# Kernel optimization log

Measured on AMD Instinct MI355X. Metric: run time of the kernel, lower is better.

Reference implementation:

```python
import jax, jax.numpy as jnp
import numpy as np

B, WK, HRS = 2048, 52, 8760
DT = 0.125          # Euler step in days (3-hourly), exactly representable
RANGE_PRED = 7      # forecast horizon in days


def setup_inputs() -> dict:
    key = jax.random.key(0)
    k1, k2, k3, k4 = jax.random.split(key, 4)
    # X_in: [B, weeks, 5, 1]; channel 0 = start time in days (same across batch,
    # the torch code reads X_in[0, week, 0, 0]); channels 1..4 = N,P,Z,D init.
    X_in = jax.random.uniform(k1, (B, WK, 5, 1), jnp.float32, 0.1, 3.0)
    t0 = jnp.arange(WK, dtype=jnp.float32) * 7.0
    X_in = X_in.at[:, :, 0, 0].set(jnp.broadcast_to(t0, (B, WK)))
    global_f = jax.random.uniform(k2, (B, HRS), jnp.float32)          # light forcing in [0,1]
    global_m = jax.random.uniform(k3, (B, HRS), jnp.float32) * 0.1    # mixing rate, small
    params_value = jax.random.uniform(k4, (B, 10), jnp.float32, 0.1, 1.0)
    return {"X_in": X_in, "global_f": global_f, "global_m": global_m,
            "params_value": params_value, "dt": DT, "range_pred": RANGE_PRED}


def reference(X_in, global_f, global_m, params_value, dt, range_pred):
    # Fixed multipliers from the torch code
    pv = jnp.asarray([1.0, 2.0, 0.1, 0.05, 0.1, 0.3, 0.6, 0.15, 0.4, 0.1], X_in.dtype)
    Q0, Vm, thr = 8.0, 1.0, 0.01  # Q0 = 4 + 2.5 + 1.5 + 0
    chi, rho, gam, lam, eps, alp, bet, eta, phi, zet = [params_value[:, i][:, None] for i in range(10)]  # [B,1]

    n_steps = int(round(range_pred / dt))      # 56
    stride = int(round(1.0 / dt))              # 8 -> daily sampling of output

    # Hourly forcing gather: same time axis for every batch element (torch uses X_in[0,...])
    t0 = X_in[0, :, 0, 0]                                                     # [W]
    times = t0[:, None] + jnp.arange(n_steps + 1, dtype=X_in.dtype) * dt      # [W, S]
    idx = jnp.round(times * 24.0).astype(jnp.int32)
    f = jnp.take(global_f, idx, axis=1)[:, :, :n_steps]                       # [B, W, T]
    m = jnp.take(global_m, idx, axis=1)[:, :, :n_steps]

    def step(carry, ft_mt):
        N, P, Z, D = carry                      # each [B, W]
        ft, mt = ft_mt
        Pc = jnp.maximum(thr, P)
        Zc = jnp.maximum(thr, Z)
        gN = N / (chi * pv[0] + N)
        zg = rho * pv[1] * (1.0 - jnp.exp(-lam * pv[3] * Pc)) * Zc
        up = Vm * gN * ft * Pc
        Nn = N + dt * (-up + alp * pv[5] * zg + eps * pv[4] * P + gam * pv[2] * Z + phi * pv[8] * D + mt * (Q0 - N))
        Pn = P + dt * (up - zg - eps * pv[4] * P - eta * pv[7] * P - mt * P)
        Zn = Z + dt * (bet * pv[6] * zg - gam * pv[2] * Z - mt * Z)
        Dn = D + dt * (eta * pv[7] * P + (1.0 - alp * pv[5] - bet * pv[6]) * zg - phi * pv[8] * D - zet * pv[9] * D - mt * D)
        new = (Nn, Pn, Zn, Dn)
        return new, jnp.stack(new, axis=0)      # [4, B, W]

    carry0 = (X_in[:, :, 1, 0], X_in[:, :, 2, 0], X_in[:, :, 3, 0], X_in[:, :, 4, 0])
    _, ys = jax.lax.scan(step, carry0, (jnp.moveaxis(f, 2, 0), jnp.moveaxis(m, 2, 0)))  # ys: [T, 4, B, W]
    traj = jnp.concatenate([jnp.stack(carry0, axis=0)[None], ys], axis=0)               # [S, 4, B, W]
    out = jnp.moveaxis(traj, (0, 1), (3, 2))                                            # [B, W, 4, S]
    return out[:, :, :, ::stride]               # daily samples: [B, W, 4, range_pred+1]
```

## Files before the change

kernel.cpp:

```cpp
#include <hip/hip_runtime.h>
#include <hip/hip_bf16.h>


typedef float f32x4 __attribute__((ext_vector_type(4)));

#define NPZD_B 2048
#define NPZD_WK 52
#define NPZD_HRS 8760
#define NPZD_NSTEPS 56
#define NPZD_NF4 2190
#define NPZD_WSTRIDE 60
#define NPZD_LDSW (NPZD_WK * NPZD_WSTRIDE + 16)

__global__ __launch_bounds__(256) void npzd_kernel(
    const float* __restrict__ X_in,
    const float* __restrict__ gf,
    const float* __restrict__ gm,
    const float* __restrict__ params,
    const float* __restrict__ dt_ptr,
    float* __restrict__ out)
{
    __shared__ __align__(16) float lds_f[NPZD_LDSW];
    __shared__ __align__(16) float lds_m[NPZD_LDSW];

    const int b   = blockIdx.x;
    const int tid = threadIdx.x;

    const f32x4* __restrict__ gf4 = (const f32x4*)(gf + (size_t)b * NPZD_HRS);
    const f32x4* __restrict__ gm4 = (const f32x4*)(gm + (size_t)b * NPZD_HRS);

    f32x4 fv[9], mv[9];
    int kk[9];
    #pragma unroll
    for (int i = 0; i < 9; ++i) {
        int k = i * 256 + tid;
        if (k >= NPZD_NF4) k = NPZD_NF4 - 1;
        kk[i] = k;
        fv[i] = __builtin_nontemporal_load(gf4 + k);
        mv[i] = __builtin_nontemporal_load(gm4 + k);
    }

    #pragma unroll
    for (int i = 0; i < 9; ++i) {
        const int k = kk[i];
        const float fe[4] = {fv[i].x, fv[i].y, fv[i].z, fv[i].w};
        const float me[4] = {mv[i].x, mv[i].y, mv[i].z, mv[i].w};
        const int rm = k % 3;
        const int e0 = (rm == 0) ? 0 : (3 - rm);
        const int j0 = (4 * k + e0) / 3;
        const int p0 = j0 + 4 * ((j0 * 9363) >> 19);
        lds_f[p0] = fe[e0];
        lds_m[p0] = me[e0];
        if (rm == 0) {
            const int j1 = j0 + 1;
            const int p1 = j1 + 4 * ((j1 * 9363) >> 19);
            lds_f[p1] = fe[3];
            lds_m[p1] = me[3];
        }
    }
    __syncthreads();

    if (tid >= NPZD_WK) return;
    const int w = tid;

    const float dt = dt_ptr[0];

    const float* xb = X_in + ((size_t)b * NPZD_WK + w) * 5;
    float N = xb[1], P = xb[2], Z = xb[3], D = xb[4];

    const float* pp = params + (size_t)b * 10;
    const float chi   = pp[0];
    const float rho2  = pp[1] * 2.0f;
    const float gam1  = pp[2] * 0.1f;
    const float lam05 = pp[3] * 0.05f;
    const float eps1  = pp[4] * 0.1f;
    const float alp3  = pp[5] * 0.3f;
    const float bet6  = pp[6] * 0.6f;
    const float eta15 = pp[7] * 0.15f;
    const float phi4  = pp[8] * 0.4f;
    const float zet1  = pp[9] * 0.1f;
    const float rem   = 1.0f - alp3 - bet6;

    float oN[8], oP[8], oZ[8], oD[8];
    oN[0] = N; oP[0] = P; oZ[0] = Z; oD[0] = D;

    const float* lf = lds_f + w * NPZD_WSTRIDE;
    const float* lm = lds_m + w * NPZD_WSTRIDE;

    #pragma unroll
    for (int g = 0; g < 14; ++g) {
        const f32x4 f4 = *(const f32x4*)(lf + 4 * g);
        const f32x4 m4 = *(const f32x4*)(lm + 4 * g);
        const float fs[4] = {f4.x, f4.y, f4.z, f4.w};
        const float ms[4] = {m4.x, m4.y, m4.z, m4.w};
        #pragma unroll
        for (int q = 0; q < 4; ++q) {
            const float ft = fs[q], mt = ms[q];
            const float Pc = fmaxf(0.01f, P);
            const float Zc = fmaxf(0.01f, Z);
            const float gN = N * __builtin_amdgcn_rcpf(chi + N);
            const float zg = rho2 * (1.0f - __expf(-lam05 * Pc)) * Zc;
            const float up = gN * ft * Pc;
            const float Nn = N + dt * (-up + alp3 * zg + eps1 * P + gam1 * Z + phi4 * D + mt * (8.0f - N));
            const float Pn = P + dt * (up - zg - eps1 * P - eta15 * P - mt * P);
            const float Zn = Z + dt * (bet6 * zg - gam1 * Z - mt * Z);
            const float Dn = D + dt * (eta15 * P + rem * zg - phi4 * D - zet1 * D - mt * D);
            N = Nn; P = Pn; Z = Zn; D = Dn;
        }
        if (g & 1) {
            const int c = (g >> 1) + 1;
            oN[c] = N; oP[c] = P; oZ[c] = Z; oD[c] = D;
        }
    }

    f32x4* o4 = (f32x4*)(out + ((size_t)b * NPZD_WK + w) * 32);
    o4[0] = (f32x4){oN[0], oN[1], oN[2], oN[3]};
    o4[1] = (f32x4){oN[4], oN[5], oN[6], oN[7]};
    o4[2] = (f32x4){oP[0], oP[1], oP[2], oP[3]};
    o4[3] = (f32x4){oP[4], oP[5], oP[6], oP[7]};
    o4[4] = (f32x4){oZ[0], oZ[1], oZ[2], oZ[3]};
    o4[5] = (f32x4){oZ[4], oZ[5], oZ[6], oZ[7]};
    o4[6] = (f32x4){oD[0], oD[1], oD[2], oD[3]};
    o4[7] = (f32x4){oD[4], oD[5], oD[6], oD[7]};
}

extern "C" void kernel_launch(void* const* d_in, const int* in_sizes, int n_in,
                              void* d_out, int out_size, void* d_ws, size_t ws_size,
                              hipStream_t stream) {
    const float* X_in   = (const float*)d_in[0];
    const float* gf     = (const float*)d_in[1];
    const float* gm     = (const float*)d_in[2];
    const float* params = (const float*)d_in[3];
    const float* dt_ptr = (const float*)d_in[4];
    float* out = (float*)d_out;

    npzd_kernel<<<NPZD_B, 256, 0, stream>>>(X_in, gf, gm, params, dt_ptr, out);
}
```

Baseline: 171.2 us.

## Warp-specialize blocks to overlap forcing loads with integration across batches

Each block now handles two batch rows. Warps 1-3 act as producers that load the next row's forcing data into registers while warp 0 integrates the current row from shared memory. Producers also load contiguous 48-byte groups and write one vector per group to shared memory instead of scattered scalar stores. This is meant to hide global-load latency behind the serial ODE loop. In exchange it halves the grid size, and the register staging may raise register pressure under the added occupancy hint.

```diff
diff --git a/kernel.cpp b/kernel.cpp
--- a/kernel.cpp
+++ b/kernel.cpp
@@ -1,5 +1,4 @@
 #include <hip/hip_runtime.h>
-#include <hip/hip_bf16.h>
 
 
 typedef float f32x4 __attribute__((ext_vector_type(4)));
@@ -7,12 +6,12 @@
 #define NPZD_B 2048
 #define NPZD_WK 52
 #define NPZD_HRS 8760
-#define NPZD_NSTEPS 56
-#define NPZD_NF4 2190
 #define NPZD_WSTRIDE 60
 #define NPZD_LDSW (NPZD_WK * NPZD_WSTRIDE + 16)
+#define NPZD_NGRP 728
+#define NPZD_BPB 2
 
-__global__ __launch_bounds__(256) void npzd_kernel(
+__global__ __launch_bounds__(256, 4) void npzd_kernel(
     const float* __restrict__ X_in,
     const float* __restrict__ gf,
     const float* __restrict__ gm,
@@ -23,105 +22,107 @@
     __shared__ __align__(16) float lds_f[NPZD_LDSW];
     __shared__ __align__(16) float lds_m[NPZD_LDSW];
 
-    const int b   = blockIdx.x;
     const int tid = threadIdx.x;
+    const int b0  = blockIdx.x * NPZD_BPB;
+    const float dt = dt_ptr[0];
 
-    const f32x4* __restrict__ gf4 = (const f32x4*)(gf + (size_t)b * NPZD_HRS);
-    const f32x4* __restrict__ gm4 = (const f32x4*)(gm + (size_t)b * NPZD_HRS);
-
-    f32x4 fv[9], mv[9];
-    int kk[9];
-    #pragma unroll
-    for (int i = 0; i < 9; ++i) {
-        int k = i * 256 + tid;
-        if (k >= NPZD_NF4) k = NPZD_NF4 - 1;
-        kk[i] = k;
-        fv[i] = __builtin_nontemporal_load(gf4 + k);
-        mv[i] = __builtin_nontemporal_load(gm4 + k);
-    }
+    f32x4 sf[4][3], sm[4][3];
+    int gg[4];
 
     #pragma unroll
-    for (int i = 0; i < 9; ++i) {
-        const int k = kk[i];
-        const float fe[4] = {fv[i].x, fv[i].y, fv[i].z, fv[i].w};
-        const float me[4] = {mv[i].x, mv[i].y, mv[i].z, mv[i].w};
-        const int rm = k % 3;
-        const int e0 = (rm == 0) ? 0 : (3 - rm);
-        const int j0 = (4 * k + e0) / 3;
-        const int p0 = j0 + 4 * ((j0 * 9363) >> 19);
-        lds_f[p0] = fe[e0];
-        lds_m[p0] = me[e0];
-        if (rm == 0) {
-            const int j1 = j0 + 1;
-            const int p1 = j1 + 4 * ((j1 * 9363) >> 19);
-            lds_f[p1] = fe[3];
-            lds_m[p1] = me[3];
+    for (int it = 0; it <= NPZD_BPB; ++it) {
+        if (it < NPZD_BPB && tid >= 64) {
+            const f32x4* __restrict__ gf4 = (const f32x4*)(gf + (size_t)(b0 + it) * NPZD_HRS);
+            const f32x4* __restrict__ gm4 = (const f32x4*)(gm + (size_t)(b0 + it) * NPZD_HRS);
+            #pragma unroll
+            for (int i = 0; i < 4; ++i) {
+                int g = (tid - 64) + 192 * i;
+                if (g >= NPZD_NGRP) g = NPZD_NGRP - 1;
+                gg[i] = g;
+                #pragma unroll
+                for (int c = 0; c < 3; ++c) {
+                    sf[i][c] = gf4[3 * g + c];
+                    sm[i][c] = gm4[3 * g + c];
+                }
+            }
         }
+
+        if (it > 0 && tid < NPZD_WK) {
+            const int b = b0 + it - 1;
+            const int w = tid;
+
+            const float* xb = X_in + ((size_t)b * NPZD_WK + w) * 5;
+            float N = xb[1], P = xb[2], Z = xb[3], D = xb[4];
+
+            const float* pp = params + (size_t)b * 10;
+            const float chi   = pp[0];
+            const float rho2  = pp[1] * 2.0f;
+            const float gam1  = pp[2] * 0.1f;
+            const float lam05 = pp[3] * 0.05f;
+            const float eps1  = pp[4] * 0.1f;
+            const float alp3  = pp[5] * 0.3f;
+            const float bet6  = pp[6] * 0.6f;
+            const float eta15 = pp[7] * 0.15f;
+            const float phi4  = pp[8] * 0.4f;
+            const float zet1  = pp[9] * 0.1f;
+            const float rem   = 1.0f - alp3 - bet6;
+
+            float oN[8], oP[8], oZ[8], oD[8];
+            oN[0] = N; oP[0] = P; oZ[0] = Z; oD[0] = D;
+
+            const float* lf = lds_f + w * NPZD_WSTRIDE;
+            const float* lm = lds_m + w * NPZD_WSTRIDE;
+
+            #pragma unroll
+            for (int g14 = 0; g14 < 14; ++g14) {
+                const f32x4 f4 = *(const f32x4*)(lf + 4 * g14);
+                const f32x4 m4 = *(const f32x4*)(lm + 4 * g14);
+                const float fs[4] = {f4.x, f4.y, f4.z, f4.w};
+                const float ms[4] = {m4.x, m4.y, m4.z, m4.w};
+                #pragma unroll
+                for (int q = 0; q < 4; ++q) {
+                    const float ft = fs[q], mt = ms[q];
+                    const float Pc = fmaxf(0.01f, P);
+                    const float Zc = fmaxf(0.01f, Z);
+                    const float gN = N * __builtin_amdgcn_rcpf(chi + N);
+                    const float zg = rho2 * (1.0f - __expf(-lam05 * Pc)) * Zc;
+                    const float up = gN * ft * Pc;
+                    const float Nn = N + dt * (-up + alp3 * zg + eps1 * P + gam1 * Z + phi4 * D + mt * (8.0f - N));
+                    const float Pn = P + dt * (up - zg - eps1 * P - eta15 * P - mt * P);
+                    const float Zn = Z + dt * (bet6 * zg - gam1 * Z - mt * Z);
+                    const float Dn = D + dt * (eta15 * P + rem * zg - phi4 * D - zet1 * D - mt * D);
+                    N = Nn; P = Pn; Z = Zn; D = Dn;
+                }
+                if (g14 & 1) {
+                    const int c = (g14 >> 1) + 1;
+                    oN[c] = N; oP[c] = P; oZ[c] = Z; oD[c] = D;
+                }
+            }
+
+            f32x4* o4 = (f32x4*)(out + ((size_t)b * NPZD_WK + w) * 32);
+            o4[0] = (f32x4){oN[0], oN[1], oN[2], oN[3]};
+            o4[1] = (f32x4){oN[4], oN[5], oN[6], oN[7]};
+            o4[2] = (f32x4){oP[0], oP[1], oP[2], oP[3]};
+            o4[3] = (f32x4){oP[4], oP[5], oP[6], oP[7]};
+            o4[4] = (f32x4){oZ[0], oZ[1], oZ[2], oZ[3]};
+            o4[5] = (f32x4){oZ[4], oZ[5], oZ[6], oZ[7]};
+            o4[6] = (f32x4){oD[0], oD[1], oD[2], oD[3]};
+            o4[7] = (f32x4){oD[4], oD[5], oD[6], oD[7]};
+        }
+        __syncthreads();
+
+        if (it < NPZD_BPB && tid >= 64) {
+            #pragma unroll
+            for (int i = 0; i < 4; ++i) {
+                const int g  = gg[i];
+                const int w  = (g * 9363) >> 17;
+                const int p0 = 4 * g + 4 * w;
+                *(f32x4*)(lds_f + p0) = (f32x4){sf[i][0].x, sf[i][0].w, sf[i][1].z, sf[i][2].y};
+                *(f32x4*)(lds_m + p0) = (f32x4){sm[i][0].x, sm[i][0].w, sm[i][1].z, sm[i][2].y};
+            }
+        }
+        __syncthreads();
     }
-    __syncthreads();
-
-    if (tid >= NPZD_WK) return;
-    const int w = tid;
-
-    const float dt = dt_ptr[0];
-
-    const float* xb = X_in + ((size_t)b * NPZD_WK + w) * 5;
-    float N = xb[1], P = xb[2], Z = xb[3], D = xb[4];
-
-    const float* pp = params + (size_t)b * 10;
-    const float chi   = pp[0];
-    const float rho2  = pp[1] * 2.0f;
-    const float gam1  = pp[2] * 0.1f;
-    const float lam05 = pp[3] * 0.05f;
-    const float eps1  = pp[4] * 0.1f;
-    const float alp3  = pp[5] * 0.3f;
-    const float bet6  = pp[6] * 0.6f;
-    const float eta15 = pp[7] * 0.15f;
-    const float phi4  = pp[8] * 0.4f;
-    const float zet1  = pp[9] * 0.1f;
-    const float rem   = 1.0f - alp3 - bet6;
-
-    float oN[8], oP[8], oZ[8], oD[8];
-    oN[0] = N; oP[0] = P; oZ[0] = Z; oD[0] = D;
-
-    const float* lf = lds_f + w * NPZD_WSTRIDE;
-    const float* lm = lds_m + w * NPZD_WSTRIDE;
-
-    #pragma unroll
-    for (int g = 0; g < 14; ++g) {
-        const f32x4 f4 = *(const f32x4*)(lf + 4 * g);
-        const f32x4 m4 = *(const f32x4*)(lm + 4 * g);
-        const float fs[4] = {f4.x, f4.y, f4.z, f4.w};
-        const float ms[4] = {m4.x, m4.y, m4.z, m4.w};
-        #pragma unroll
-        for (int q = 0; q < 4; ++q) {
-            const float ft = fs[q], mt = ms[q];
-            const float Pc = fmaxf(0.01f, P);
-            const float Zc = fmaxf(0.01f, Z);
-            const float gN = N * __builtin_amdgcn_rcpf(chi + N);
-            const float zg = rho2 * (1.0f - __expf(-lam05 * Pc)) * Zc;
-            const float up = gN * ft * Pc;
-            const float Nn = N + dt * (-up + alp3 * zg + eps1 * P + gam1 * Z + phi4 * D + mt * (8.0f - N));
-            const float Pn = P + dt * (up - zg - eps1 * P - eta15 * P - mt * P);
-            const float Zn = Z + dt * (bet6 * zg - gam1 * Z - mt * Z);
-            const float Dn = D + dt * (eta15 * P + rem * zg - phi4 * D - zet1 * D - mt * D);
-            N = Nn; P = Pn; Z = Zn; D = Dn;
-        }
-        if (g & 1) {
-            const int c = (g >> 1) + 1;
-            oN[c] = N; oP[c] = P; oZ[c] = Z; oD[c] = D;
-        }
-    }
-
-    f32x4* o4 = (f32x4*)(out + ((size_t)b * NPZD_WK + w) * 32);
-    o4[0] = (f32x4){oN[0], oN[1], oN[2], oN[3]};
-    o4[1] = (f32x4){oN[4], oN[5], oN[6], oN[7]};
-    o4[2] = (f32x4){oP[0], oP[1], oP[2], oP[3]};
-    o4[3] = (f32x4){oP[4], oP[5], oP[6], oP[7]};
-    o4[4] = (f32x4){oZ[0], oZ[1], oZ[2], oZ[3]};
-    o4[5] = (f32x4){oZ[4], oZ[5], oZ[6], oZ[7]};
-    o4[6] = (f32x4){oD[0], oD[1], oD[2], oD[3]};
-    o4[7] = (f32x4){oD[4], oD[5], oD[6], oD[7]};
 }
 
 extern "C" void kernel_launch(void* const* d_in, const int* in_sizes, int n_in,
@@ -134,5 +135,5 @@
     const float* dt_ptr = (const float*)d_in[4];
     float* out = (float*)d_out;
 
-    npzd_kernel<<<NPZD_B, 256, 0, stream>>>(X_in, gf, gm, params, dt_ptr, out);
+    npzd_kernel<<<NPZD_B / NPZD_BPB, 256, 0, stream>>>(X_in, gf, gm, params, dt_ptr, out);
 }
```

After: 184.4 us. 1.08x slower.

## Use single-wavefront blocks with four load passes and early param loads

Applied to the files above, without the earlier changes.

Blocks shrink from 256 to 64 threads, so a single wavefront does both the forcing gather into LDS (four passes of nine float4 loads) and the 52-lane time integration. This avoids leaving three idle wavefronts per block during the serial compute, and a single-wave block makes the barrier cheap. X_in and parameter loads are hoisted ahead of the gather so their latency overlaps it. Nontemporal loads are replaced by plain loads. The cost is that one wave now issues all the global loads, which may reduce memory-level parallelism per block. LDS usage per block is unchanged, so occupancy now depends on LDS relative to the much smaller blocks.

```diff
diff --git a/kernel.cpp b/kernel.cpp
--- a/kernel.cpp
+++ b/kernel.cpp
@@ -1,5 +1,4 @@
 #include <hip/hip_runtime.h>
-#include <hip/hip_bf16.h>
 
 
 typedef float f32x4 __attribute__((ext_vector_type(4)));
@@ -7,12 +6,11 @@
 #define NPZD_B 2048
 #define NPZD_WK 52
 #define NPZD_HRS 8760
-#define NPZD_NSTEPS 56
 #define NPZD_NF4 2190
 #define NPZD_WSTRIDE 60
 #define NPZD_LDSW (NPZD_WK * NPZD_WSTRIDE + 16)
 
-__global__ __launch_bounds__(256) void npzd_kernel(
+__global__ __launch_bounds__(64, 4) void npzd_kernel(
     const float* __restrict__ X_in,
     const float* __restrict__ gf,
     const float* __restrict__ gm,
@@ -23,50 +21,13 @@
     __shared__ __align__(16) float lds_f[NPZD_LDSW];
     __shared__ __align__(16) float lds_m[NPZD_LDSW];
 
-    const int b   = blockIdx.x;
-    const int tid = threadIdx.x;
-
-    const f32x4* __restrict__ gf4 = (const f32x4*)(gf + (size_t)b * NPZD_HRS);
-    const f32x4* __restrict__ gm4 = (const f32x4*)(gm + (size_t)b * NPZD_HRS);
-
-    f32x4 fv[9], mv[9];
-    int kk[9];
-    #pragma unroll
-    for (int i = 0; i < 9; ++i) {
-        int k = i * 256 + tid;
-        if (k >= NPZD_NF4) k = NPZD_NF4 - 1;
-        kk[i] = k;
-        fv[i] = __builtin_nontemporal_load(gf4 + k);
-        mv[i] = __builtin_nontemporal_load(gm4 + k);
-    }
-
-    #pragma unroll
-    for (int i = 0; i < 9; ++i) {
-        const int k = kk[i];
-        const float fe[4] = {fv[i].x, fv[i].y, fv[i].z, fv[i].w};
-        const float me[4] = {mv[i].x, mv[i].y, mv[i].z, mv[i].w};
-        const int rm = k % 3;
-        const int e0 = (rm == 0) ? 0 : (3 - rm);
-        const int j0 = (4 * k + e0) / 3;
-        const int p0 = j0 + 4 * ((j0 * 9363) >> 19);
-        lds_f[p0] = fe[e0];
-        lds_m[p0] = me[e0];
-        if (rm == 0) {
-            const int j1 = j0 + 1;
-            const int p1 = j1 + 4 * ((j1 * 9363) >> 19);
-            lds_f[p1] = fe[3];
-            lds_m[p1] = me[3];
-        }
-    }
-    __syncthreads();
-
-    if (tid >= NPZD_WK) return;
-    const int w = tid;
+    const int b    = blockIdx.x;
+    const int lane = threadIdx.x;
 
     const float dt = dt_ptr[0];
-
-    const float* xb = X_in + ((size_t)b * NPZD_WK + w) * 5;
-    float N = xb[1], P = xb[2], Z = xb[3], D = xb[4];
+    const int wc = (lane < NPZD_WK) ? lane : (NPZD_WK - 1);
+    const float* xb = X_in + ((size_t)b * NPZD_WK + wc) * 5;
+    const float x1 = xb[1], x2 = xb[2], x3 = xb[3], x4 = xb[4];
 
     const float* pp = params + (size_t)b * 10;
     const float chi   = pp[0];
@@ -80,6 +41,47 @@
     const float phi4  = pp[8] * 0.4f;
     const float zet1  = pp[9] * 0.1f;
     const float rem   = 1.0f - alp3 - bet6;
+
+    const f32x4* __restrict__ gf4 = (const f32x4*)(gf + (size_t)b * NPZD_HRS);
+    const f32x4* __restrict__ gm4 = (const f32x4*)(gm + (size_t)b * NPZD_HRS);
+
+    #pragma unroll
+    for (int pass = 0; pass < 4; ++pass) {
+        f32x4 fv[9], mv[9];
+        int kk[9];
+        #pragma unroll
+        for (int c = 0; c < 9; ++c) {
+            int k = (pass * 9 + c) * 64 + lane;
+            if (k >= NPZD_NF4) k = NPZD_NF4 - 1;
+            kk[c] = k;
+            fv[c] = gf4[k];
+            mv[c] = gm4[k];
+        }
+        #pragma unroll
+        for (int c = 0; c < 9; ++c) {
+            const int k = kk[c];
+            const float fe[4] = {fv[c].x, fv[c].y, fv[c].z, fv[c].w};
+            const float me[4] = {mv[c].x, mv[c].y, mv[c].z, mv[c].w};
+            const int rm = k % 3;
+            const int e0 = (rm == 0) ? 0 : (3 - rm);
+            const int j0 = (4 * k + e0) / 3;
+            const int p0 = j0 + 4 * ((j0 * 9363) >> 19);
+            lds_f[p0] = fe[e0];
+            lds_m[p0] = me[e0];
+            if (rm == 0) {
+                const int j1 = j0 + 1;
+                const int p1 = j1 + 4 * ((j1 * 9363) >> 19);
+                lds_f[p1] = fe[3];
+                lds_m[p1] = me[3];
+            }
+        }
+    }
+    __syncthreads();
+
+    if (lane >= NPZD_WK) return;
+    const int w = lane;
+
+    float N = x1, P = x2, Z = x3, D = x4;
 
     float oN[8], oP[8], oZ[8], oD[8];
     oN[0] = N; oP[0] = P; oZ[0] = Z; oD[0] = D;
@@ -134,5 +136,5 @@
     const float* dt_ptr = (const float*)d_in[4];
     float* out = (float*)d_out;
 
-    npzd_kernel<<<NPZD_B, 256, 0, stream>>>(X_in, gf, gm, params, dt_ptr, out);
+    npzd_kernel<<<NPZD_B, 64, 0, stream>>>(X_in, gf, gm, params, dt_ptr, out);
 }
```

Result: slower. 182.8 us (+6.8%).
